# Kernel optimization log

Hardware: AMD Instinct MI355X
Metric: run time of the kernel (lower is better)

Reference implementation:

```python
import jax, jax.numpy as jnp
import numpy as np

B = 8192          # batch_size
NB = 4096         # num_banks (== mask length)
PAD = NB // 2     # reflect pad on each side


def setup_inputs() -> dict:
    key = jax.random.key(0)
    k1, k2, k3 = jax.random.split(key, 3)
    logits = jax.random.normal(k1, (NB,), dtype=jnp.float32) * 0.1
    u = jax.random.uniform(k2, (B, NB), dtype=jnp.float32)          # Bernoulli uniforms
    shift = jax.random.randint(k3, (B,), 0, NB, dtype=jnp.int32)    # per-sample shift
    return {"logits": logits, "u": u, "shift": shift}


def reference(logits, u, shift):
    # Bernoulli(sigmoid(logits)) sample via inverse-CDF on externally supplied uniforms
    p = jax.nn.sigmoid(logits)                       # (NB,)
    grid = (u < p).astype(jnp.float32)               # (B, NB)
    # Bernoulli log_prob summed over banks: g*log(p) + (1-g)*log(1-p)
    log_probs = (grid * jax.nn.log_sigmoid(logits)
                 + (1.0 - grid) * jax.nn.log_sigmoid(-logits)).sum(axis=1)  # (B,)
    # reflect-pad along bank axis, then gather a shifted window of length NB
    padded = jnp.pad(grid, ((0, 0), (PAD, PAD)), mode="reflect")    # (B, NB+2*PAD)
    idx = shift[:, None].astype(jnp.int32) + jnp.arange(NB, dtype=jnp.int32)[None, :]
    masks = jnp.take_along_axis(padded, idx, axis=1)[:, None, :]    # (B, 1, NB)
    return masks, log_probs
```

## Files before the change

kernel.cpp:

```cpp
#include <hip/hip_runtime.h>
#include <math.h>

#define NB 4096
#define PAD 2048
#define BLOCK 256

__device__ __forceinline__ int mirror_idx(int i) {
    i = ::abs(i);
    return (i < NB) ? i : (2 * (NB - 1) - i);
}

__global__ void fbmp_precompute(const float* __restrict__ logits, float* __restrict__ ws) {
    int j = blockIdx.x * blockDim.x + threadIdx.x;
    if (j >= NB) return;
    float x = logits[j];
    double xd = (double)x;
    float e = (float)exp(-xd);
    float p = 1.0f / (1.0f + e);
    float lsp = (float)(-log1p(exp(-xd)));
    float lsn = (float)(-log1p(exp(xd)));
    ws[j] = p;
    ws[NB + j] = lsp;
    ws[2 * NB + j] = lsn;
}

__global__ __launch_bounds__(BLOCK) void fbmp_main(
    const float* __restrict__ u, const int* __restrict__ shift,
    const float* __restrict__ ws,
    float* __restrict__ masks, float* __restrict__ logp)
{
    __shared__ float sg[NB];
    __shared__ float sred[BLOCK / 64];

    const int b = blockIdx.x;
    const float4* __restrict__ u4   = (const float4*)(u + (size_t)b * NB);
    const float4* __restrict__ p4   = (const float4*)(ws);
    const float4* __restrict__ lsp4 = (const float4*)(ws + NB);
    const float4* __restrict__ lsn4 = (const float4*)(ws + 2 * NB);

    float acc = 0.0f;
    for (int i = threadIdx.x; i < NB / 4; i += BLOCK) {
        float4 uv = u4[i];
        float4 pv = p4[i];
        float4 ap = lsp4[i];
        float4 an = lsn4[i];
        bool c0 = uv.x < pv.x;
        bool c1 = uv.y < pv.y;
        bool c2 = uv.z < pv.z;
        bool c3 = uv.w < pv.w;
        acc += (c0 ? ap.x : an.x) + (c1 ? ap.y : an.y)
             + (c2 ? ap.z : an.z) + (c3 ? ap.w : an.w);
        float4 g;
        g.x = c0 ? 1.0f : 0.0f;
        g.y = c1 ? 1.0f : 0.0f;
        g.z = c2 ? 1.0f : 0.0f;
        g.w = c3 ? 1.0f : 0.0f;
        ((float4*)sg)[i] = g;
    }

    #pragma unroll
    for (int off = 32; off > 0; off >>= 1)
        acc += __shfl_down(acc, off, 64);
    const int lane = threadIdx.x & 63;
    const int wid  = threadIdx.x >> 6;
    if (lane == 0) sred[wid] = acc;
    __syncthreads();
    if (threadIdx.x == 0) {
        float t = 0.0f;
        #pragma unroll
        for (int w = 0; w < BLOCK / 64; ++w) t += sred[w];
        logp[b] = t;
    }

    const int s = shift[b] - PAD;
    float4* __restrict__ m4 = (float4*)(masks + (size_t)b * NB);
    for (int i = threadIdx.x; i < NB / 4; i += BLOCK) {
        int k = 4 * i + s;
        float4 o;
        o.x = sg[mirror_idx(k + 0)];
        o.y = sg[mirror_idx(k + 1)];
        o.z = sg[mirror_idx(k + 2)];
        o.w = sg[mirror_idx(k + 3)];
        m4[i] = o;
    }
}

extern "C" void kernel_launch(void* const* d_in, const int* in_sizes, int n_in,
                              void* d_out, int out_size, void* d_ws, size_t ws_size,
                              hipStream_t stream) {
    const float* logits = (const float*)d_in[0];
    const float* u      = (const float*)d_in[1];
    const int*   shift  = (const int*)d_in[2];
    const int B = in_sizes[2];

    float* ws    = (float*)d_ws;
    float* masks = (float*)d_out;
    float* logp  = (float*)d_out + (size_t)B * NB;

    fbmp_precompute<<<(NB + 255) / 256, 256, 0, stream>>>(logits, ws);
    fbmp_main<<<B, BLOCK, 0, stream>>>(u, shift, ws, masks, logp);
}
```

Measured before the change: 241.9 us.

## Process one row per wavefront with ballot bitmasks and LDS-cached tables

Restructures the main kernel so each 64-lane wavefront handles one batch row inside 1024-thread blocks. The sigmoid and log-sigmoid tables are copied into LDS once per block. Per-row Bernoulli results are packed into 64-bit ballot words in LDS instead of a float array, and the gather reads bits back out of those words. The per-block reduction barrier is gone, and the mask output uses nontemporal stores. In exchange, each block spends 48KB of LDS on the table copy, and the bit-extraction indexing adds ALU work.

```diff
diff --git a/kernel.cpp b/kernel.cpp
--- a/kernel.cpp
+++ b/kernel.cpp
@@ -3,7 +3,10 @@
 
 #define NB 4096
 #define PAD 2048
-#define BLOCK 256
+#define TPB 1024
+#define WPB 16
+
+typedef float f32x4 __attribute__((ext_vector_type(4)));
 
 __device__ __forceinline__ int mirror_idx(int i) {
     i = ::abs(i);
@@ -24,22 +27,42 @@
     ws[2 * NB + j] = lsn;
 }
 
-__global__ __launch_bounds__(BLOCK) void fbmp_main(
+__global__ __launch_bounds__(TPB, 4) void fbmp_wave(
     const float* __restrict__ u, const int* __restrict__ shift,
     const float* __restrict__ ws,
-    float* __restrict__ masks, float* __restrict__ logp)
+    float* __restrict__ masks, float* __restrict__ logp, int B)
 {
-    __shared__ float sg[NB];
-    __shared__ float sred[BLOCK / 64];
+    __shared__ float tbl[3 * NB];
+    __shared__ unsigned long long words[WPB][64];
 
-    const int b = blockIdx.x;
-    const float4* __restrict__ u4   = (const float4*)(u + (size_t)b * NB);
-    const float4* __restrict__ p4   = (const float4*)(ws);
-    const float4* __restrict__ lsp4 = (const float4*)(ws + NB);
-    const float4* __restrict__ lsn4 = (const float4*)(ws + 2 * NB);
+    const int t = threadIdx.x;
 
-    float acc = 0.0f;
-    for (int i = threadIdx.x; i < NB / 4; i += BLOCK) {
+    {
+        const float4* __restrict__ src = (const float4*)ws;
+        float4* __restrict__ dst = (float4*)tbl;
+        #pragma unroll
+        for (int c = 0; c < (3 * NB / 4) / TPB; ++c)
+            dst[t + c * TPB] = src[t + c * TPB];
+    }
+    __syncthreads();
+
+    const int lane = t & 63;
+    const int wid  = t >> 6;
+    const int row  = blockIdx.x * WPB + wid;
+    if (row >= B) return;
+
+    const int s = shift[row] - PAD;
+    const float4* __restrict__ u4   = (const float4*)(u + (size_t)row * NB);
+    const float4* __restrict__ p4   = (const float4*)tbl;
+    const float4* __restrict__ lsp4 = (const float4*)(tbl + NB);
+    const float4* __restrict__ lsn4 = (const float4*)(tbl + 2 * NB);
+
+    float accw[4] = {0.0f, 0.0f, 0.0f, 0.0f};
+    unsigned long long myword = 0ull;
+
+    #pragma unroll
+    for (int c = 0; c < 16; ++c) {
+        const int i = lane + 64 * c;
         float4 uv = u4[i];
         float4 pv = p4[i];
         float4 ap = lsp4[i];
@@ -48,40 +71,67 @@
         bool c1 = uv.y < pv.y;
         bool c2 = uv.z < pv.z;
         bool c3 = uv.w < pv.w;
-        acc += (c0 ? ap.x : an.x) + (c1 ? ap.y : an.y)
-             + (c2 ? ap.z : an.z) + (c3 ? ap.w : an.w);
-        float4 g;
-        g.x = c0 ? 1.0f : 0.0f;
-        g.y = c1 ? 1.0f : 0.0f;
-        g.z = c2 ? 1.0f : 0.0f;
-        g.w = c3 ? 1.0f : 0.0f;
-        ((float4*)sg)[i] = g;
+        accw[c & 3] += (c0 ? ap.x : an.x) + (c1 ? ap.y : an.y)
+                     + (c2 ? ap.z : an.z) + (c3 ? ap.w : an.w);
+        unsigned long long b0 = __ballot(c0);
+        unsigned long long b1 = __ballot(c1);
+        unsigned long long b2 = __ballot(c2);
+        unsigned long long b3 = __ballot(c3);
+        if ((lane >> 2) == c) {
+            unsigned long long m0 = (lane & 1) ? b1 : b0;
+            unsigned long long m1 = (lane & 1) ? b3 : b2;
+            myword = (lane & 2) ? m1 : m0;
+        }
+    }
+    words[wid][lane] = myword;
+
+    #pragma unroll
+    for (int w = 0; w < 4; ++w) {
+        #pragma unroll
+        for (int off = 32; off > 0; off >>= 1)
+            accw[w] += __shfl_down(accw[w], off, 64);
+    }
+    if (lane == 0) {
+        float tt = 0.0f;
+        tt += accw[0];
+        tt += accw[1];
+        tt += accw[2];
+        tt += accw[3];
+        logp[row] = tt;
     }
 
+    const unsigned int* __restrict__ w32 = (const unsigned int*)&words[wid][0];
+    float* __restrict__ mrow = masks + (size_t)row * NB;
     #pragma unroll
-    for (int off = 32; off > 0; off >>= 1)
-        acc += __shfl_down(acc, off, 64);
-    const int lane = threadIdx.x & 63;
-    const int wid  = threadIdx.x >> 6;
-    if (lane == 0) sred[wid] = acc;
-    __syncthreads();
-    if (threadIdx.x == 0) {
-        float t = 0.0f;
-        #pragma unroll
-        for (int w = 0; w < BLOCK / 64; ++w) t += sred[w];
-        logp[b] = t;
-    }
-
-    const int s = shift[b] - PAD;
-    float4* __restrict__ m4 = (float4*)(masks + (size_t)b * NB);
-    for (int i = threadIdx.x; i < NB / 4; i += BLOCK) {
-        int k = 4 * i + s;
-        float4 o;
-        o.x = sg[mirror_idx(k + 0)];
-        o.y = sg[mirror_idx(k + 1)];
-        o.z = sg[mirror_idx(k + 2)];
-        o.w = sg[mirror_idx(k + 3)];
-        m4[i] = o;
+    for (int c = 0; c < 16; ++c) {
+        const int i = lane + 64 * c;
+        const int k = 4 * i + s;
+        f32x4 o;
+        {
+            const int j = mirror_idx(k + 0);
+            const int w64 = ((j >> 8) << 2) | (j & 3);
+            const int bit = (j >> 2) & 63;
+            o.x = ((w32[(w64 << 1) | (bit >> 5)] >> (bit & 31)) & 1u) ? 1.0f : 0.0f;
+        }
+        {
+            const int j = mirror_idx(k + 1);
+            const int w64 = ((j >> 8) << 2) | (j & 3);
+            const int bit = (j >> 2) & 63;
+            o.y = ((w32[(w64 << 1) | (bit >> 5)] >> (bit & 31)) & 1u) ? 1.0f : 0.0f;
+        }
+        {
+            const int j = mirror_idx(k + 2);
+            const int w64 = ((j >> 8) << 2) | (j & 3);
+            const int bit = (j >> 2) & 63;
+            o.z = ((w32[(w64 << 1) | (bit >> 5)] >> (bit & 31)) & 1u) ? 1.0f : 0.0f;
+        }
+        {
+            const int j = mirror_idx(k + 3);
+            const int w64 = ((j >> 8) << 2) | (j & 3);
+            const int bit = (j >> 2) & 63;
+            o.w = ((w32[(w64 << 1) | (bit >> 5)] >> (bit & 31)) & 1u) ? 1.0f : 0.0f;
+        }
+        __builtin_nontemporal_store(o, (f32x4*)mrow + i);
     }
 }
 
@@ -98,5 +148,6 @@
     float* logp  = (float*)d_out + (size_t)B * NB;
 
     fbmp_precompute<<<(NB + 255) / 256, 256, 0, stream>>>(logits, ws);
-    fbmp_main<<<B, BLOCK, 0, stream>>>(u, shift, ws, masks, logp);
+    const int grid = (B + WPB - 1) / WPB;
+    fbmp_wave<<<grid, TPB, 0, stream>>>(u, shift, ws, masks, logp, B);
 }
```

After: 249.9 us. 3.3% more time.

## Process rows per wavefront with register double-buffered loads and bit-packed masks

Applied to the files above, without the earlier changes.

Each wavefront now handles four rows. The next row's uniforms are prefetched into registers while the current row is processed, and the grid is stored as 64-bit ballot words in shared memory instead of a float array. Probability and log-sigmoid tables are staged in LDS once per block, and mask outputs use nontemporal stores. This removes block-wide syncs per row and cuts LDS traffic, at the cost of heavy register use (32 float4 buffers) and possible lower occupancy.

```diff
diff --git a/kernel.cpp b/kernel.cpp
--- a/kernel.cpp
+++ b/kernel.cpp
@@ -3,7 +3,10 @@
 
 #define NB 4096
 #define PAD 2048
-#define BLOCK 256
+#define TPB 256
+#define RPW 4
+
+typedef float f32x4 __attribute__((ext_vector_type(4)));
 
 __device__ __forceinline__ int mirror_idx(int i) {
     i = ::abs(i);
@@ -24,65 +27,140 @@
     ws[2 * NB + j] = lsn;
 }
 
-__global__ __launch_bounds__(BLOCK) void fbmp_main(
+#define PIPE_ROW(R, C, N, S)                                                   \
+  if ((R) < myrows) {                                                          \
+    const int row = base + (R);                                                \
+    if ((R) + 1 < myrows) {                                                    \
+      const float4* __restrict__ nr4 =                                         \
+          (const float4*)(u + (size_t)(row + 1) * NB);                         \
+      _Pragma("unroll")                                                        \
+      for (int c = 0; c < 16; ++c) N[c] = nr4[lane + 64 * c];                  \
+    }                                                                          \
+    float accw0 = 0.f, accw1 = 0.f, accw2 = 0.f, accw3 = 0.f;                  \
+    unsigned long long myword = 0ull;                                          \
+    _Pragma("unroll")                                                          \
+    for (int c = 0; c < 16; ++c) {                                             \
+      const int i = lane + 64 * c;                                             \
+      float4 pv = p4[i];                                                       \
+      float4 ap = lsp4[i];                                                     \
+      float4 an = lsn4[i];                                                     \
+      bool c0 = C[c].x < pv.x;                                                 \
+      bool c1 = C[c].y < pv.y;                                                 \
+      bool c2 = C[c].z < pv.z;                                                 \
+      bool c3 = C[c].w < pv.w;                                                 \
+      float term = (c0 ? ap.x : an.x) + (c1 ? ap.y : an.y)                     \
+                 + (c2 ? ap.z : an.z) + (c3 ? ap.w : an.w);                    \
+      if ((c & 3) == 0) accw0 += term;                                         \
+      else if ((c & 3) == 1) accw1 += term;                                    \
+      else if ((c & 3) == 2) accw2 += term;                                    \
+      else accw3 += term;                                                      \
+      unsigned long long b0 = __ballot(c0);                                    \
+      unsigned long long b1 = __ballot(c1);                                    \
+      unsigned long long b2 = __ballot(c2);                                    \
+      unsigned long long b3 = __ballot(c3);                                    \
+      if ((lane >> 2) == c) {                                                  \
+        unsigned long long m0 = (lane & 1) ? b1 : b0;                          \
+        unsigned long long m1 = (lane & 1) ? b3 : b2;                          \
+        myword = (lane & 2) ? m1 : m0;                                         \
+      }                                                                        \
+    }                                                                          \
+    words[wid][lane] = myword;                                                 \
+    _Pragma("unroll")                                                          \
+    for (int off = 32; off > 0; off >>= 1) {                                   \
+      accw0 += __shfl_down(accw0, off, 64);                                    \
+      accw1 += __shfl_down(accw1, off, 64);                                    \
+      accw2 += __shfl_down(accw2, off, 64);                                    \
+      accw3 += __shfl_down(accw3, off, 64);                                    \
+    }                                                                          \
+    if (lane == 0) {                                                           \
+      float tt = 0.0f;                                                         \
+      tt += accw0;                                                             \
+      tt += accw1;                                                             \
+      tt += accw2;                                                             \
+      tt += accw3;                                                             \
+      logp[row] = tt;                                                          \
+    }                                                                          \
+    const unsigned int* __restrict__ w32 =                                     \
+        (const unsigned int*)&words[wid][0];                                   \
+    float* __restrict__ mrow = masks + (size_t)row * NB;                       \
+    _Pragma("unroll")                                                          \
+    for (int c = 0; c < 16; ++c) {                                             \
+      const int i = lane + 64 * c;                                             \
+      const int k = 4 * i + (S);                                               \
+      f32x4 o;                                                                 \
+      {                                                                        \
+        const int j = mirror_idx(k + 0);                                       \
+        const int w64 = ((j >> 8) << 2) | (j & 3);                             \
+        const int bit = (j >> 2) & 63;                                         \
+        o.x = ((w32[(w64 << 1) | (bit >> 5)] >> (bit & 31)) & 1u) ? 1.0f : 0.0f; \
+      }                                                                        \
+      {                                                                        \
+        const int j = mirror_idx(k + 1);                                       \
+        const int w64 = ((j >> 8) << 2) | (j & 3);                             \
+        const int bit = (j >> 2) & 63;                                         \
+        o.y = ((w32[(w64 << 1) | (bit >> 5)] >> (bit & 31)) & 1u) ? 1.0f : 0.0f; \
+      }                                                                        \
+      {                                                                        \
+        const int j = mirror_idx(k + 2);                                       \
+        const int w64 = ((j >> 8) << 2) | (j & 3);                             \
+        const int bit = (j >> 2) & 63;                                         \
+        o.z = ((w32[(w64 << 1) | (bit >> 5)] >> (bit & 31)) & 1u) ? 1.0f : 0.0f; \
+      }                                                                        \
+      {                                                                        \
+        const int j = mirror_idx(k + 3);                                       \
+        const int w64 = ((j >> 8) << 2) | (j & 3);                             \
+        const int bit = (j >> 2) & 63;                                         \
+        o.w = ((w32[(w64 << 1) | (bit >> 5)] >> (bit & 31)) & 1u) ? 1.0f : 0.0f; \
+      }                                                                        \
+      __builtin_nontemporal_store(o, (f32x4*)mrow + i);                        \
+    }                                                                          \
+  }
+
+__global__ __launch_bounds__(TPB, 2) void fbmp_pipe(
     const float* __restrict__ u, const int* __restrict__ shift,
     const float* __restrict__ ws,
-    float* __restrict__ masks, float* __restrict__ logp)
+    float* __restrict__ masks, float* __restrict__ logp, int B)
 {
-    __shared__ float sg[NB];
-    __shared__ float sred[BLOCK / 64];
+    __shared__ float tbl[3 * NB];
+    __shared__ unsigned long long words[TPB / 64][64];
 
-    const int b = blockIdx.x;
-    const float4* __restrict__ u4   = (const float4*)(u + (size_t)b * NB);
-    const float4* __restrict__ p4   = (const float4*)(ws);
-    const float4* __restrict__ lsp4 = (const float4*)(ws + NB);
-    const float4* __restrict__ lsn4 = (const float4*)(ws + 2 * NB);
+    const int t = threadIdx.x;
+    {
+        const float4* __restrict__ src = (const float4*)ws;
+        float4* __restrict__ dst = (float4*)tbl;
+        #pragma unroll
+        for (int c = 0; c < (3 * NB / 4) / TPB; ++c)
+            dst[t + c * TPB] = src[t + c * TPB];
+    }
+    __syncthreads();
 
-    float acc = 0.0f;
-    for (int i = threadIdx.x; i < NB / 4; i += BLOCK) {
-        float4 uv = u4[i];
-        float4 pv = p4[i];
-        float4 ap = lsp4[i];
-        float4 an = lsn4[i];
-        bool c0 = uv.x < pv.x;
-        bool c1 = uv.y < pv.y;
-        bool c2 = uv.z < pv.z;
-        bool c3 = uv.w < pv.w;
-        acc += (c0 ? ap.x : an.x) + (c1 ? ap.y : an.y)
-             + (c2 ? ap.z : an.z) + (c3 ? ap.w : an.w);
-        float4 g;
-        g.x = c0 ? 1.0f : 0.0f;
-        g.y = c1 ? 1.0f : 0.0f;
-        g.z = c2 ? 1.0f : 0.0f;
-        g.w = c3 ? 1.0f : 0.0f;
-        ((float4*)sg)[i] = g;
+    const int lane = t & 63;
+    const int wid  = t >> 6;
+    const int gw   = blockIdx.x * (TPB / 64) + wid;
+    const int base = gw * RPW;
+    if (base >= B) return;
+    const int myrows = (B - base < RPW) ? (B - base) : RPW;
+
+    const float4* __restrict__ p4   = (const float4*)tbl;
+    const float4* __restrict__ lsp4 = (const float4*)(tbl + NB);
+    const float4* __restrict__ lsn4 = (const float4*)(tbl + 2 * NB);
+
+    const int s0 = shift[base] - PAD;
+    const int s1 = (myrows > 1) ? shift[base + 1] - PAD : 0;
+    const int s2 = (myrows > 2) ? shift[base + 2] - PAD : 0;
+    const int s3 = (myrows > 3) ? shift[base + 3] - PAD : 0;
+
+    float4 bufA[16], bufB[16];
+    {
+        const float4* __restrict__ r4 = (const float4*)(u + (size_t)base * NB);
+        #pragma unroll
+        for (int c = 0; c < 16; ++c) bufA[c] = r4[lane + 64 * c];
     }
 
-    #pragma unroll
-    for (int off = 32; off > 0; off >>= 1)
-        acc += __shfl_down(acc, off, 64);
-    const int lane = threadIdx.x & 63;
-    const int wid  = threadIdx.x >> 6;
-    if (lane == 0) sred[wid] = acc;
-    __syncthreads();
-    if (threadIdx.x == 0) {
-        float t = 0.0f;
-        #pragma unroll
-        for (int w = 0; w < BLOCK / 64; ++w) t += sred[w];
-        logp[b] = t;
-    }
-
-    const int s = shift[b] - PAD;
-    float4* __restrict__ m4 = (float4*)(masks + (size_t)b * NB);
-    for (int i = threadIdx.x; i < NB / 4; i += BLOCK) {
-        int k = 4 * i + s;
-        float4 o;
-        o.x = sg[mirror_idx(k + 0)];
-        o.y = sg[mirror_idx(k + 1)];
-        o.z = sg[mirror_idx(k + 2)];
-        o.w = sg[mirror_idx(k + 3)];
-        m4[i] = o;
-    }
+    PIPE_ROW(0, bufA, bufB, s0)
+    PIPE_ROW(1, bufB, bufA, s1)
+    PIPE_ROW(2, bufA, bufB, s2)
+    PIPE_ROW(3, bufB, bufA, s3)
 }
 
 extern "C" void kernel_launch(void* const* d_in, const int* in_sizes, int n_in,
@@ -98,5 +176,8 @@
     float* logp  = (float*)d_out + (size_t)B * NB;
 
     fbmp_precompute<<<(NB + 255) / 256, 256, 0, stream>>>(logits, ws);
-    fbmp_main<<<B, BLOCK, 0, stream>>>(u, shift, ws, masks, logp);
+
+    const int waves = (B + RPW - 1) / RPW;
+    const int grid  = (waves + (TPB / 64) - 1) / (TPB / 64);
+    fbmp_pipe<<<grid, TPB, 0, stream>>>(u, shift, ws, masks, logp, B);
 }
```

New measurement: 274.0 us. +13.2%, slower.
